# Kernel optimization log

Hardware: AMD Instinct MI355X
Metric: run time of the kernel (lower is better)

Reference implementation:

```python
import jax, jax.numpy as jnp
import numpy as np

NUM_JOINTS = 32
N_E = 1024
E_DIM = 128
BETA = 0.25
HID = 256
CHAINS = [[0,1,2,3,4,5],[0,6,7,8,9,10],[0,11,12,13,14,15],
          [12,16,17,18,19,20,21,22,23],[12,24,25,26,27,28,29,30,31]]


def setup_inputs() -> dict:
    key = jax.random.key(0)
    ks = jax.random.split(key, 8)
    B, T = 64, 128
    z = jax.random.normal(ks[0], (B, T, NUM_JOINTS, E_DIM), jnp.float32)
    # xavier_uniform for embeddings: bound = sqrt(6/(n_e+e_dim))
    eb = float(np.sqrt(6.0 / (N_E + E_DIM)))
    emb = jax.random.uniform(ks[1], (NUM_JOINTS, N_E, E_DIM), jnp.float32, -eb, eb)
    # torch Linear default init: U(-1/sqrt(fan_in), 1/sqrt(fan_in))
    b1b = float(1.0 / np.sqrt(2 * E_DIM))
    W1 = jax.random.uniform(ks[2], (2 * E_DIM, HID), jnp.float32, -b1b, b1b)
    b1 = jax.random.uniform(ks[3], (HID,), jnp.float32, -b1b, b1b)
    ln_g = jnp.ones((HID,), jnp.float32)
    ln_b = jnp.zeros((HID,), jnp.float32)
    b2b = float(1.0 / np.sqrt(HID))
    W2 = jax.random.uniform(ks[4], (HID, E_DIM), jnp.float32, -b2b, b2b)
    b2 = jax.random.uniform(ks[5], (E_DIM,), jnp.float32, -b2b, b2b)
    return {"z": z, "emb": emb, "W1": W1, "b1": b1, "ln_g": ln_g,
            "ln_b": ln_b, "W2": W2, "b2": b2}


def _layernorm(x, g, b, eps=1e-5):
    m = jnp.mean(x, axis=-1, keepdims=True)
    v = jnp.mean((x - m) ** 2, axis=-1, keepdims=True)
    return (x - m) * jax.lax.rsqrt(v + eps) * g + b


def _mlp(x, W1, b1, ln_g, ln_b, W2, b2):
    h = x @ W1 + b1
    h = jax.nn.relu(_layernorm(h, ln_g, ln_b))
    return h @ W2 + b2


def _quantize_joint(h, E):
    # h: [B,T,C], E: [n_e,C]. argmin of euclidean dist == argmin of -2 h.E^T + |E|^2
    B, T, C = h.shape
    hf = h.reshape(-1, C)
    d = -2.0 * (hf @ E.T) + jnp.sum(E * E, axis=1)  # [B*T, n_e]
    idx = jnp.argmin(d, axis=1)
    e = E[idx].reshape(B, T, C)  # one-hot @ E == gather
    sg = jax.lax.stop_gradient
    loss = jnp.mean((sg(e) - h) ** 2) + BETA * jnp.mean((e - sg(h)) ** 2)
    q = h + sg(e - h)  # straight-through
    return q, e, idx.reshape(B, T), loss


def reference(z, emb, W1, b1, ln_g, ln_b, W2, b2):
    B, T, V, C = z.shape
    sg = jax.lax.stop_gradient
    stored_q, stored_e, stored_idx = {}, {}, {}
    total = jnp.zeros((), z.dtype)
    for chain in CHAINS:
        parent_e = None
        for i, j in enumerate(chain):
            if j not in stored_q:  # single-pass per joint
                zj = z[:, :, j, :]
                h = _mlp(jnp.concatenate([parent_e, zj], -1), W1, b1, ln_g, ln_b, W2, b2) if i > 0 else zj
                q, e, idx, loss = _quantize_joint(h, emb[j])
                stored_q[j], stored_e[j], stored_idx[j] = q, e, idx
                total = total + loss
            parent_e = sg(stored_e[j])
    z_q = jnp.stack([stored_q[v] for v in range(V)], axis=2)      # [B,T,V,C]
    indices = jnp.stack([stored_idx[v] for v in range(V)], axis=2)  # [B,T,V]
    return z_q, total / V, indices
```

## Files before the change

### kernel.cpp

```cpp
#include <hip/hip_runtime.h>

#define NJ 32
#define NE 1024
#define CD 128
#define HID 256
#define ROWS 8192
#define RB 64
#define BPJ (ROWS / RB)

struct Lv { int nj; int j[5]; int p[5]; };

__global__ __launch_bounds__(256) void norms_kernel(const float* __restrict__ emb,
                                                    float* __restrict__ nrm) {
  int gid = blockIdx.x * 256 + threadIdx.x;
  int n = gid >> 2, l = gid & 3;
  const float* row = emb + (size_t)n * CD;
  float s = 0.f;
#pragma unroll
  for (int i = 0; i < 8; ++i) {
    float4 v = *(const float4*)&row[(l + 4 * i) * 4];
    s += v.x * v.x + v.y * v.y + v.z * v.z + v.w * v.w;
  }
  s += __shfl_xor(s, 1);
  s += __shfl_xor(s, 2);
  if (l == 0) nrm[n] = s;
}

__global__ __launch_bounds__(256) void fused_level(
    const float* __restrict__ z, const float* __restrict__ emb,
    const float* __restrict__ W1, const float* __restrict__ b1,
    const float* __restrict__ lng, const float* __restrict__ lnb,
    const float* __restrict__ W2, const float* __restrict__ b2,
    const float* __restrict__ nrm,
    float* __restrict__ zq, float* __restrict__ idx_out,
    float* __restrict__ partials, Lv lv, int pbase) {
  __shared__ __align__(16) float smem[19520];
  __shared__ float wsum[4];
  float* hs  = smem;
  float* S   = smem + 8704;
  float* xs  = S;
  float* ws1 = S + 2176;
  float* as_ = S;
  float* ws2 = S + 8704;
  float* es  = S;
  float* nsm = S + 8256;

  const int tid = threadIdx.x;
  const int rg = tid >> 5, cg = tid & 31;
  const int u = cg & 15;
  const int qcA = (cg >> 4) * 128 + u * 4;
  const int qcB = qcA + 64;
  const int jl = blockIdx.x / BPJ;
  const int row0 = (blockIdx.x % BPJ) * RB;
  const int jj = lv.j[jl], pj = lv.p[jl];
  const size_t rstride = (size_t)NJ * CD;

  if (pj >= 0) {
    float acc1[8][8];
#pragma unroll
    for (int r = 0; r < 8; ++r)
#pragma unroll
      for (int c = 0; c < 8; ++c) acc1[r][c] = 0.f;

#pragma unroll 1
    for (int ks = 0; ks < 8; ++ks) {
#pragma unroll
      for (int uu = 0; uu < 2; ++uu) {
        int idx = uu * 256 + tid;
        int r = idx >> 3, kq = idx & 7;
        const float* src = (ks < 4)
            ? (zq + (size_t)(row0 + r) * rstride + (size_t)pj * CD + (ks * 32 + kq * 4))
            : (z  + (size_t)(row0 + r) * rstride + (size_t)jj * CD + (ks * 32 - 128 + kq * 4));
        float4 v = *(const float4*)src;
        xs[(kq * 4 + 0) * 68 + r] = v.x;
        xs[(kq * 4 + 1) * 68 + r] = v.y;
        xs[(kq * 4 + 2) * 68 + r] = v.z;
        xs[(kq * 4 + 3) * 68 + r] = v.w;
      }
#pragma unroll
      for (int v8 = 0; v8 < 8; ++v8) {
        int idx = v8 * 256 + tid;
        int k = idx >> 6, c4 = idx & 63;
        *(float4*)&ws1[k * 264 + c4 * 4] =
            *(const float4*)&W1[(size_t)(ks * 32 + k) * HID + c4 * 4];
      }
      __syncthreads();
#pragma unroll 2
      for (int kk = 0; kk < 32; ++kk) {
        float xr[8], wc[8];
        *(float4*)&xr[0] = *(const float4*)&xs[kk * 68 + rg * 8];
        *(float4*)&xr[4] = *(const float4*)&xs[kk * 68 + rg * 8 + 4];
        *(float4*)&wc[0] = *(const float4*)&ws1[kk * 264 + qcA];
        *(float4*)&wc[4] = *(const float4*)&ws1[kk * 264 + qcB];
#pragma unroll
        for (int r = 0; r < 8; ++r)
#pragma unroll
          for (int c = 0; c < 8; ++c)
            acc1[r][c] += xr[r] * wc[c];
      }
      __syncthreads();
    }

    {
      float bb[8], gg[8], be[8];
      *(float4*)&bb[0] = *(const float4*)&b1[qcA];
      *(float4*)&bb[4] = *(const float4*)&b1[qcB];
      *(float4*)&gg[0] = *(const float4*)&lng[qcA];
      *(float4*)&gg[4] = *(const float4*)&lng[qcB];
      *(float4*)&be[0] = *(const float4*)&lnb[qcA];
      *(float4*)&be[4] = *(const float4*)&lnb[qcB];
#pragma unroll
      for (int r = 0; r < 8; ++r) {
        float s0 = 0.f, q0 = 0.f;
#pragma unroll
        for (int j = 0; j < 8; ++j) {
          float v = acc1[r][j] + bb[j];
          acc1[r][j] = v;
          s0 += v; q0 += v * v;
        }
        float si = __shfl_xor(s0, 16), qi = __shfl_xor(q0, 16);
        float s1 = si, q1 = qi;
#pragma unroll
        for (int j = 0; j < 8; ++j) {
          float v = acc1[r][j];
          s1 += v; q1 += v * v;
        }
#pragma unroll
        for (int m = 1; m < 16; m <<= 1) {
          s1 += __shfl_xor(s1, m); q1 += __shfl_xor(q1, m);
        }
        float s2 = __shfl_xor(s1, 16), q2 = __shfl_xor(q1, 16);
        float Sx = (cg & 16) ? s1 : s2;
        float Qx = (cg & 16) ? q1 : q2;
        float mu = Sx * (1.f / HID);
        float va = Qx * (1.f / HID) - mu * mu;
        float iv = 1.f / sqrtf(va + 1e-5f);
#pragma unroll
        for (int j = 0; j < 8; ++j) {
          float a = (acc1[r][j] - mu) * iv * gg[j] + be[j];
          acc1[r][j] = fmaxf(a, 0.f);
        }
      }
    }

    float acc2[8][4];
#pragma unroll
    for (int r = 0; r < 8; ++r)
#pragma unroll
      for (int c = 0; c < 4; ++c) acc2[r][c] = 0.f;

#pragma unroll 1
    for (int half = 0; half < 2; ++half) {
      __syncthreads();
      if ((cg >> 4) == half) {
#pragma unroll
        for (int j = 0; j < 8; ++j) {
          int kl = (j >> 2) * 64 + u * 4 + (j & 3);
          *(float4*)&as_[kl * 68 + rg * 8] =
              make_float4(acc1[0][j], acc1[1][j], acc1[2][j], acc1[3][j]);
          *(float4*)&as_[kl * 68 + rg * 8 + 4] =
              make_float4(acc1[4][j], acc1[5][j], acc1[6][j], acc1[7][j]);
        }
      }
      __syncthreads();
#pragma unroll 1
      for (int kc = 0; kc < 8; ++kc) {
#pragma unroll
        for (int v = 0; v < 2; ++v) {
          int idx = v * 256 + tid;
          int k = idx >> 5, c4 = idx & 31;
          *(float4*)&ws2[k * 132 + c4 * 4] =
              *(const float4*)&W2[(size_t)(half * 128 + kc * 16 + k) * CD + c4 * 4];
        }
        __syncthreads();
#pragma unroll 2
        for (int kk = 0; kk < 16; ++kk) {
          float ar[8], wc2[4];
          *(float4*)&ar[0] = *(const float4*)&as_[(kc * 16 + kk) * 68 + rg * 8];
          *(float4*)&ar[4] = *(const float4*)&as_[(kc * 16 + kk) * 68 + rg * 8 + 4];
          *(float4*)&wc2[0] = *(const float4*)&ws2[kk * 132 + cg * 4];
#pragma unroll
          for (int r = 0; r < 8; ++r)
#pragma unroll
            for (int c = 0; c < 4; ++c)
              acc2[r][c] += ar[r] * wc2[c];
        }
        __syncthreads();
      }
    }
    {
      float4 bv = *(const float4*)&b2[cg * 4];
      float bb2[4] = {bv.x, bv.y, bv.z, bv.w};
#pragma unroll
      for (int c = 0; c < 4; ++c) {
        float4 lo = make_float4(acc2[0][c] + bb2[c], acc2[1][c] + bb2[c],
                                acc2[2][c] + bb2[c], acc2[3][c] + bb2[c]);
        float4 hi = make_float4(acc2[4][c] + bb2[c], acc2[5][c] + bb2[c],
                                acc2[6][c] + bb2[c], acc2[7][c] + bb2[c]);
        *(float4*)&hs[(cg * 4 + c) * 68 + rg * 8] = lo;
        *(float4*)&hs[(cg * 4 + c) * 68 + rg * 8 + 4] = hi;
      }
    }
  } else {
#pragma unroll
    for (int v = 0; v < 8; ++v) {
      int idx = v * 256 + tid;
      int r = idx >> 5, c4 = idx & 31;
      float4 vz = *(const float4*)&z[(size_t)(row0 + r) * rstride + (size_t)jj * CD + c4 * 4];
      hs[(c4 * 4 + 0) * 68 + r] = vz.x;
      hs[(c4 * 4 + 1) * 68 + r] = vz.y;
      hs[(c4 * 4 + 2) * 68 + r] = vz.z;
      hs[(c4 * 4 + 3) * 68 + r] = vz.w;
    }
  }

  float mnv[8]; int mni[8];
#pragma unroll
  for (int r = 0; r < 8; ++r) { mnv[r] = 3.402823e38f; mni[r] = 0; }
  const float* embJ = emb + (size_t)jj * NE * CD;
  const float* nrmJ = nrm + jj * NE;

#pragma unroll 1
  for (int p = 0; p < 2; ++p) {
    __syncthreads();
    if (tid < 128) {
      *(float4*)&nsm[tid * 4] = *(const float4*)&nrmJ[p * 512 + tid * 4];
    }
    float acc4[8][16];
#pragma unroll
    for (int r = 0; r < 8; ++r)
#pragma unroll
      for (int c = 0; c < 16; ++c) acc4[r][c] = 0.f;

#pragma unroll 1
    for (int kc = 0; kc < 8; ++kc) {
#pragma unroll
      for (int v = 0; v < 8; ++v) {
        int idx = v * 256 + tid;
        int n = idx >> 2, kq = idx & 3;
        float4 ev = *(const float4*)&embJ[(size_t)(p * 512 + n) * CD + kc * 16 + kq * 4];
        es[(kq * 4 + 0) * 516 + n] = ev.x;
        es[(kq * 4 + 1) * 516 + n] = ev.y;
        es[(kq * 4 + 2) * 516 + n] = ev.z;
        es[(kq * 4 + 3) * 516 + n] = ev.w;
      }
      __syncthreads();
#pragma unroll 2
      for (int kk = 0; kk < 16; ++kk) {
        int c = kc * 16 + kk;
        float hr[8], ec[16];
        *(float4*)&hr[0] = *(const float4*)&hs[c * 68 + rg * 8];
        *(float4*)&hr[4] = *(const float4*)&hs[c * 68 + rg * 8 + 4];
        *(float4*)&ec[0]  = *(const float4*)&es[kk * 516 + qcA];
        *(float4*)&ec[4]  = *(const float4*)&es[kk * 516 + qcB];
        *(float4*)&ec[8]  = *(const float4*)&es[kk * 516 + 256 + qcA];
        *(float4*)&ec[12] = *(const float4*)&es[kk * 516 + 256 + qcB];
#pragma unroll
        for (int r = 0; r < 8; ++r)
#pragma unroll
          for (int c2 = 0; c2 < 16; ++c2)
            acc4[r][c2] += hr[r] * ec[c2];
      }
      __syncthreads();
    }
#pragma unroll
    for (int r = 0; r < 8; ++r) {
#pragma unroll
      for (int q = 0; q < 4; ++q) {
        int o = ((q & 1) ? qcB : qcA) + (q >> 1) * 256;
#pragma unroll
        for (int cc = 0; cc < 4; ++cc) {
          int nl = o + cc;
          float d = nsm[nl] - 2.f * acc4[r][q * 4 + cc];
          int n = p * 512 + nl;
          if (d < mnv[r]) { mnv[r] = d; mni[r] = n; }
        }
      }
    }
  }

#pragma unroll
  for (int r = 0; r < 8; ++r) {
    float mv = mnv[r]; int mi = mni[r];
#pragma unroll
    for (int m = 1; m < 32; m <<= 1) {
      float om = __shfl_xor(mv, m); int oi = __shfl_xor(mi, m);
      if (om < mv || (om == mv && oi < mi)) { mv = om; mi = oi; }
    }
    mnv[r] = mv; mni[r] = mi;
  }

  float lsum = 0.f;
#pragma unroll
  for (int r = 0; r < 8; ++r) {
    int row = rg * 8 + r;
    int id = mni[r];
    const float* erow = embJ + (size_t)id * CD;
    float4 ev = *(const float4*)&erow[cg * 4];
    float h0 = hs[(cg * 4 + 0) * 68 + row];
    float h1 = hs[(cg * 4 + 1) * 68 + row];
    float h2 = hs[(cg * 4 + 2) * 68 + row];
    float h3 = hs[(cg * 4 + 3) * 68 + row];
    float dx = ev.x - h0, dy = ev.y - h1, dz = ev.z - h2, dw = ev.w - h3;
    lsum += dx * dx + dy * dy + dz * dz + dw * dw;
    *(float4*)&zq[(size_t)(row0 + row) * rstride + (size_t)jj * CD + cg * 4] = ev;
    if (cg == 0) idx_out[(size_t)(row0 + row) * NJ + jj] = (float)id;
  }
#pragma unroll
  for (int m = 1; m < 64; m <<= 1) lsum += __shfl_xor(lsum, m);
  if ((tid & 63) == 0) wsum[tid >> 6] = lsum;
  __syncthreads();
  if (tid == 0) partials[pbase + blockIdx.x] = wsum[0] + wsum[1] + wsum[2] + wsum[3];
}

__global__ __launch_bounds__(256) void loss_reduce(const float* __restrict__ p, int n,
                                                   float* __restrict__ out) {
  __shared__ float ws[4];
  float s = 0.f;
  for (int i = threadIdx.x; i < n; i += 256) s += p[i];
#pragma unroll
  for (int m = 1; m < 64; m <<= 1) s += __shfl_xor(s, m);
  if ((threadIdx.x & 63) == 0) ws[threadIdx.x >> 6] = s;
  __syncthreads();
  if (threadIdx.x == 0)
    out[0] = (ws[0] + ws[1] + ws[2] + ws[3]) * (1.25f / (1048576.f * 32.f));
}

extern "C" void kernel_launch(void* const* d_in, const int* in_sizes, int n_in,
                              void* d_out, int out_size, void* d_ws, size_t ws_size,
                              hipStream_t stream) {
  const float* z = (const float*)d_in[0];
  const float* emb = (const float*)d_in[1];
  const float* W1 = (const float*)d_in[2];
  const float* b1 = (const float*)d_in[3];
  const float* lng = (const float*)d_in[4];
  const float* lnb = (const float*)d_in[5];
  const float* W2 = (const float*)d_in[6];
  const float* b2 = (const float*)d_in[7];

  float* zq = (float*)d_out;
  float* loss = zq + (size_t)ROWS * NJ * CD;
  float* idxo = loss + 1;

  float* nrm = (float*)d_ws;
  float* partials = nrm + NJ * NE;

  norms_kernel<<<NJ * NE * 4 / 256, 256, 0, stream>>>(emb, nrm);

  static const Lv levels[11] = {
      {1, {0, 0, 0, 0, 0}, {-1, 0, 0, 0, 0}},
      {3, {1, 6, 11, 0, 0}, {0, 0, 0, 0, 0}},
      {3, {2, 7, 12, 0, 0}, {1, 6, 11, 0, 0}},
      {5, {3, 8, 13, 16, 24}, {2, 7, 12, 12, 12}},
      {5, {4, 9, 14, 17, 25}, {3, 8, 13, 16, 24}},
      {5, {5, 10, 15, 18, 26}, {4, 9, 14, 17, 25}},
      {2, {19, 27, 0, 0, 0}, {18, 26, 0, 0, 0}},
      {2, {20, 28, 0, 0, 0}, {19, 27, 0, 0, 0}},
      {2, {21, 29, 0, 0, 0}, {20, 28, 0, 0, 0}},
      {2, {22, 30, 0, 0, 0}, {21, 29, 0, 0, 0}},
      {2, {23, 31, 0, 0, 0}, {22, 30, 0, 0, 0}},
  };

  int pbase = 0;
  for (int L = 0; L < 11; ++L) {
    fused_level<<<levels[L].nj * BPJ, 256, 0, stream>>>(
        z, emb, W1, b1, lng, lnb, W2, b2, nrm, zq, idxo, partials, levels[L], pbase);
    pbase += levels[L].nj * BPJ;
  }
  loss_reduce<<<1, 256, 0, stream>>>(partials, pbase, loss);
}
```

Before: 1.944 ms.

## Templatize row-block size and use smaller blocks on low-joint levels

The fused per-level kernel becomes a template over rows per block (32 or 64), with the shared-memory layout resized to match. Levels with only one or two joints use 32-row blocks to double the grid and fill more CUs. Occupancy hints are added to the launch bounds. The codebook staging chunk shrinks from 16 to 8 dimensions to cut LDS use, at the cost of more barriers and smaller per-thread tiles on the 32-row variant.

```diff
diff --git a/kernel.cpp b/kernel.cpp
--- a/kernel.cpp
+++ b/kernel.cpp
@@ -5,8 +5,6 @@
 #define CD 128
 #define HID 256
 #define ROWS 8192
-#define RB 64
-#define BPJ (ROWS / RB)
 
 struct Lv { int nj; int j[5]; int p[5]; };
 
@@ -26,7 +24,8 @@
   if (l == 0) nrm[n] = s;
 }
 
-__global__ __launch_bounds__(256) void fused_level(
+template <int RB>
+__global__ __launch_bounds__(256, RB == 32 ? 4 : 3) void fused_level(
     const float* __restrict__ z, const float* __restrict__ emb,
     const float* __restrict__ W1, const float* __restrict__ b1,
     const float* __restrict__ lng, const float* __restrict__ lnb,
@@ -34,16 +33,26 @@
     const float* __restrict__ nrm,
     float* __restrict__ zq, float* __restrict__ idx_out,
     float* __restrict__ partials, Lv lv, int pbase) {
-  __shared__ __align__(16) float smem[19520];
+  constexpr int RPG = RB / 8;
+  constexpr int HSP = RB + 4;
+  constexpr int BPJ = ROWS / RB;
+  constexpr int XS_SZ = 32 * HSP;
+  constexpr int HS_SZ = 128 * HSP;
+  constexpr int P1 = XS_SZ + 8448;
+  constexpr int P3 = HS_SZ + 2112;
+  constexpr int P4 = HS_SZ + 4128 + 512;
+  constexpr int SM12 = (P1 > P3) ? P1 : P3;
+  constexpr int SMEM = (SM12 > P4) ? SM12 : P4;
+
+  __shared__ __align__(16) float smem[SMEM];
   __shared__ float wsum[4];
+  float* xs  = smem;
+  float* ws1 = smem + XS_SZ;
+  float* as_ = smem;
+  float* ws2 = smem + HS_SZ;
   float* hs  = smem;
-  float* S   = smem + 8704;
-  float* xs  = S;
-  float* ws1 = S + 2176;
-  float* as_ = S;
-  float* ws2 = S + 8704;
-  float* es  = S;
-  float* nsm = S + 8256;
+  float* es  = smem + HS_SZ;
+  float* nsm = smem + HS_SZ + 4128;
 
   const int tid = threadIdx.x;
   const int rg = tid >> 5, cg = tid & 31;
@@ -56,26 +65,26 @@
   const size_t rstride = (size_t)NJ * CD;
 
   if (pj >= 0) {
-    float acc1[8][8];
-#pragma unroll
-    for (int r = 0; r < 8; ++r)
+    float acc1[RPG][8];
+#pragma unroll
+    for (int r = 0; r < RPG; ++r)
 #pragma unroll
       for (int c = 0; c < 8; ++c) acc1[r][c] = 0.f;
 
 #pragma unroll 1
     for (int ks = 0; ks < 8; ++ks) {
 #pragma unroll
-      for (int uu = 0; uu < 2; ++uu) {
+      for (int uu = 0; uu < RB / 32; ++uu) {
         int idx = uu * 256 + tid;
         int r = idx >> 3, kq = idx & 7;
         const float* src = (ks < 4)
             ? (zq + (size_t)(row0 + r) * rstride + (size_t)pj * CD + (ks * 32 + kq * 4))
             : (z  + (size_t)(row0 + r) * rstride + (size_t)jj * CD + (ks * 32 - 128 + kq * 4));
         float4 v = *(const float4*)src;
-        xs[(kq * 4 + 0) * 68 + r] = v.x;
-        xs[(kq * 4 + 1) * 68 + r] = v.y;
-        xs[(kq * 4 + 2) * 68 + r] = v.z;
-        xs[(kq * 4 + 3) * 68 + r] = v.w;
+        xs[(kq * 4 + 0) * HSP + r] = v.x;
+        xs[(kq * 4 + 1) * HSP + r] = v.y;
+        xs[(kq * 4 + 2) * HSP + r] = v.z;
+        xs[(kq * 4 + 3) * HSP + r] = v.w;
       }
 #pragma unroll
       for (int v8 = 0; v8 < 8; ++v8) {
@@ -87,13 +96,14 @@
       __syncthreads();
 #pragma unroll 2
       for (int kk = 0; kk < 32; ++kk) {
-        float xr[8], wc[8];
-        *(float4*)&xr[0] = *(const float4*)&xs[kk * 68 + rg * 8];
-        *(float4*)&xr[4] = *(const float4*)&xs[kk * 68 + rg * 8 + 4];
+        float xr[RPG], wc[8];
+#pragma unroll
+        for (int g = 0; g < RPG / 4; ++g)
+          *(float4*)&xr[g * 4] = *(const float4*)&xs[kk * HSP + rg * RPG + g * 4];
         *(float4*)&wc[0] = *(const float4*)&ws1[kk * 264 + qcA];
         *(float4*)&wc[4] = *(const float4*)&ws1[kk * 264 + qcB];
 #pragma unroll
-        for (int r = 0; r < 8; ++r)
+        for (int r = 0; r < RPG; ++r)
 #pragma unroll
           for (int c = 0; c < 8; ++c)
             acc1[r][c] += xr[r] * wc[c];
@@ -110,7 +120,7 @@
       *(float4*)&be[0] = *(const float4*)&lnb[qcA];
       *(float4*)&be[4] = *(const float4*)&lnb[qcB];
 #pragma unroll
-      for (int r = 0; r < 8; ++r) {
+      for (int r = 0; r < RPG; ++r) {
         float s0 = 0.f, q0 = 0.f;
 #pragma unroll
         for (int j = 0; j < 8; ++j) {
@@ -143,9 +153,9 @@
       }
     }
 
-    float acc2[8][4];
-#pragma unroll
-    for (int r = 0; r < 8; ++r)
+    float acc2[RPG][4];
+#pragma unroll
+    for (int r = 0; r < RPG; ++r)
 #pragma unroll
       for (int c = 0; c < 4; ++c) acc2[r][c] = 0.f;
 
@@ -156,10 +166,11 @@
 #pragma unroll
         for (int j = 0; j < 8; ++j) {
           int kl = (j >> 2) * 64 + u * 4 + (j & 3);
-          *(float4*)&as_[kl * 68 + rg * 8] =
-              make_float4(acc1[0][j], acc1[1][j], acc1[2][j], acc1[3][j]);
-          *(float4*)&as_[kl * 68 + rg * 8 + 4] =
-              make_float4(acc1[4][j], acc1[5][j], acc1[6][j], acc1[7][j]);
+#pragma unroll
+          for (int g = 0; g < RPG / 4; ++g)
+            *(float4*)&as_[kl * HSP + rg * RPG + g * 4] =
+                make_float4(acc1[g * 4 + 0][j], acc1[g * 4 + 1][j],
+                            acc1[g * 4 + 2][j], acc1[g * 4 + 3][j]);
         }
       }
       __syncthreads();
@@ -175,12 +186,14 @@
         __syncthreads();
 #pragma unroll 2
         for (int kk = 0; kk < 16; ++kk) {
-          float ar[8], wc2[4];
-          *(float4*)&ar[0] = *(const float4*)&as_[(kc * 16 + kk) * 68 + rg * 8];
-          *(float4*)&ar[4] = *(const float4*)&as_[(kc * 16 + kk) * 68 + rg * 8 + 4];
+          float ar[RPG], wc2[4];
+#pragma unroll
+          for (int g = 0; g < RPG / 4; ++g)
+            *(float4*)&ar[g * 4] =
+                *(const float4*)&as_[(kc * 16 + kk) * HSP + rg * RPG + g * 4];
           *(float4*)&wc2[0] = *(const float4*)&ws2[kk * 132 + cg * 4];
 #pragma unroll
-          for (int r = 0; r < 8; ++r)
+          for (int r = 0; r < RPG; ++r)
 #pragma unroll
             for (int c = 0; c < 4; ++c)
               acc2[r][c] += ar[r] * wc2[c];
@@ -193,30 +206,29 @@
       float bb2[4] = {bv.x, bv.y, bv.z, bv.w};
 #pragma unroll
       for (int c = 0; c < 4; ++c) {
-        float4 lo = make_float4(acc2[0][c] + bb2[c], acc2[1][c] + bb2[c],
-                                acc2[2][c] + bb2[c], acc2[3][c] + bb2[c]);
-        float4 hi = make_float4(acc2[4][c] + bb2[c], acc2[5][c] + bb2[c],
-                                acc2[6][c] + bb2[c], acc2[7][c] + bb2[c]);
-        *(float4*)&hs[(cg * 4 + c) * 68 + rg * 8] = lo;
-        *(float4*)&hs[(cg * 4 + c) * 68 + rg * 8 + 4] = hi;
+#pragma unroll
+        for (int g = 0; g < RPG / 4; ++g)
+          *(float4*)&hs[(cg * 4 + c) * HSP + rg * RPG + g * 4] =
+              make_float4(acc2[g * 4 + 0][c] + bb2[c], acc2[g * 4 + 1][c] + bb2[c],
+                          acc2[g * 4 + 2][c] + bb2[c], acc2[g * 4 + 3][c] + bb2[c]);
       }
     }
   } else {
 #pragma unroll
-    for (int v = 0; v < 8; ++v) {
+    for (int v = 0; v < RB / 8; ++v) {
       int idx = v * 256 + tid;
       int r = idx >> 5, c4 = idx & 31;
       float4 vz = *(const float4*)&z[(size_t)(row0 + r) * rstride + (size_t)jj * CD + c4 * 4];
-      hs[(c4 * 4 + 0) * 68 + r] = vz.x;
-      hs[(c4 * 4 + 1) * 68 + r] = vz.y;
-      hs[(c4 * 4 + 2) * 68 + r] = vz.z;
-      hs[(c4 * 4 + 3) * 68 + r] = vz.w;
-    }
-  }
-
-  float mnv[8]; int mni[8];
-#pragma unroll
-  for (int r = 0; r < 8; ++r) { mnv[r] = 3.402823e38f; mni[r] = 0; }
+      hs[(c4 * 4 + 0) * HSP + r] = vz.x;
+      hs[(c4 * 4 + 1) * HSP + r] = vz.y;
+      hs[(c4 * 4 + 2) * HSP + r] = vz.z;
+      hs[(c4 * 4 + 3) * HSP + r] = vz.w;
+    }
+  }
+
+  float mnv[RPG]; int mni[RPG];
+#pragma unroll
+  for (int r = 0; r < RPG; ++r) { mnv[r] = 3.402823e38f; mni[r] = 0; }
   const float* embJ = emb + (size_t)jj * NE * CD;
   const float* nrmJ = nrm + jj * NE;
 
@@ -226,19 +238,19 @@
     if (tid < 128) {
       *(float4*)&nsm[tid * 4] = *(const float4*)&nrmJ[p * 512 + tid * 4];
     }
-    float acc4[8][16];
-#pragma unroll
-    for (int r = 0; r < 8; ++r)
+    float acc4[RPG][16];
+#pragma unroll
+    for (int r = 0; r < RPG; ++r)
 #pragma unroll
       for (int c = 0; c < 16; ++c) acc4[r][c] = 0.f;
 
 #pragma unroll 1
-    for (int kc = 0; kc < 8; ++kc) {
-#pragma unroll
-      for (int v = 0; v < 8; ++v) {
+    for (int kc = 0; kc < 16; ++kc) {
+#pragma unroll
+      for (int v = 0; v < 4; ++v) {
         int idx = v * 256 + tid;
-        int n = idx >> 2, kq = idx & 3;
-        float4 ev = *(const float4*)&embJ[(size_t)(p * 512 + n) * CD + kc * 16 + kq * 4];
+        int n = idx >> 1, kq = idx & 1;
+        float4 ev = *(const float4*)&embJ[(size_t)(p * 512 + n) * CD + kc * 8 + kq * 4];
         es[(kq * 4 + 0) * 516 + n] = ev.x;
         es[(kq * 4 + 1) * 516 + n] = ev.y;
         es[(kq * 4 + 2) * 516 + n] = ev.z;
@@ -246,17 +258,18 @@
       }
       __syncthreads();
 #pragma unroll 2
-      for (int kk = 0; kk < 16; ++kk) {
-        int c = kc * 16 + kk;
-        float hr[8], ec[16];
-        *(float4*)&hr[0] = *(const float4*)&hs[c * 68 + rg * 8];
-        *(float4*)&hr[4] = *(const float4*)&hs[c * 68 + rg * 8 + 4];
+      for (int kk = 0; kk < 8; ++kk) {
+        int c = kc * 8 + kk;
+        float hr[RPG], ec[16];
+#pragma unroll
+        for (int g = 0; g < RPG / 4; ++g)
+          *(float4*)&hr[g * 4] = *(const float4*)&hs[c * HSP + rg * RPG + g * 4];
         *(float4*)&ec[0]  = *(const float4*)&es[kk * 516 + qcA];
         *(float4*)&ec[4]  = *(const float4*)&es[kk * 516 + qcB];
         *(float4*)&ec[8]  = *(const float4*)&es[kk * 516 + 256 + qcA];
         *(float4*)&ec[12] = *(const float4*)&es[kk * 516 + 256 + qcB];
 #pragma unroll
-        for (int r = 0; r < 8; ++r)
+        for (int r = 0; r < RPG; ++r)
 #pragma unroll
           for (int c2 = 0; c2 < 16; ++c2)
             acc4[r][c2] += hr[r] * ec[c2];
@@ -264,7 +277,7 @@
       __syncthreads();
     }
 #pragma unroll
-    for (int r = 0; r < 8; ++r) {
+    for (int r = 0; r < RPG; ++r) {
 #pragma unroll
       for (int q = 0; q < 4; ++q) {
         int o = ((q & 1) ? qcB : qcA) + (q >> 1) * 256;
@@ -280,7 +293,7 @@
   }
 
 #pragma unroll
-  for (int r = 0; r < 8; ++r) {
+  for (int r = 0; r < RPG; ++r) {
     float mv = mnv[r]; int mi = mni[r];
 #pragma unroll
     for (int m = 1; m < 32; m <<= 1) {
@@ -292,15 +305,15 @@
 
   float lsum = 0.f;
 #pragma unroll
-  for (int r = 0; r < 8; ++r) {
-    int row = rg * 8 + r;
+  for (int r = 0; r < RPG; ++r) {
+    int row = rg * RPG + r;
     int id = mni[r];
     const float* erow = embJ + (size_t)id * CD;
     float4 ev = *(const float4*)&erow[cg * 4];
-    float h0 = hs[(cg * 4 + 0) * 68 + row];
-    float h1 = hs[(cg * 4 + 1) * 68 + row];
-    float h2 = hs[(cg * 4 + 2) * 68 + row];
-    float h3 = hs[(cg * 4 + 3) * 68 + row];
+    float h0 = hs[(cg * 4 + 0) * HSP + row];
+    float h1 = hs[(cg * 4 + 1) * HSP + row];
+    float h2 = hs[(cg * 4 + 2) * HSP + row];
+    float h3 = hs[(cg * 4 + 3) * HSP + row];
     float dx = ev.x - h0, dy = ev.y - h1, dz = ev.z - h2, dw = ev.w - h3;
     lsum += dx * dx + dy * dy + dz * dz + dw * dw;
     *(float4*)&zq[(size_t)(row0 + row) * rstride + (size_t)jj * CD + cg * 4] = ev;
@@ -360,12 +373,20 @@
       {2, {22, 30, 0, 0, 0}, {21, 29, 0, 0, 0}},
       {2, {23, 31, 0, 0, 0}, {22, 30, 0, 0, 0}},
   };
+  static const int rbs[11] = {32, 64, 64, 64, 64, 64, 32, 32, 32, 32, 32};
 
   int pbase = 0;
   for (int L = 0; L < 11; ++L) {
-    fused_level<<<levels[L].nj * BPJ, 256, 0, stream>>>(
-        z, emb, W1, b1, lng, lnb, W2, b2, nrm, zq, idxo, partials, levels[L], pbase);
-    pbase += levels[L].nj * BPJ;
+    int bpj = ROWS / rbs[L];
+    int blocks = levels[L].nj * bpj;
+    if (rbs[L] == 64) {
+      fused_level<64><<<blocks, 256, 0, stream>>>(
+          z, emb, W1, b1, lng, lnb, W2, b2, nrm, zq, idxo, partials, levels[L], pbase);
+    } else {
+      fused_level<32><<<blocks, 256, 0, stream>>>(
+          z, emb, W1, b1, lng, lnb, W2, b2, nrm, zq, idxo, partials, levels[L], pbase);
+    }
+    pbase += blocks;
   }
   loss_reduce<<<1, 256, 0, stream>>>(partials, pbase, loss);
 }
```

After: 2.106 ms. 8.3% more time.
